# Optimization experiments

Measured on AMD Instinct MI355X. Metric: run time of the kernel, lower is better.

Reference implementation:

```python
import jax, jax.numpy as jnp
import numpy as np

A, B, NB = 100_000, 200_000, 6      # atoms, directed bonds, max neighbors
FA, FB, H = 133, 147, 256            # atom fdim, bond fdim, hidden
M, DEPTH = 5_000, 4                  # molecules, message-passing depth


def setup_inputs() -> dict:
    key = jax.random.key(0)
    ks = jax.random.split(key, 12)
    f_atoms = jax.random.normal(ks[0], (A, FA), jnp.float32)
    f_bonds = jax.random.normal(ks[1], (B, FB), jnp.float32)
    a2b = jax.random.randint(ks[2], (A, NB), 0, B, dtype=jnp.int32)
    b2a = jax.random.randint(ks[3], (B,), 0, A, dtype=jnp.int32)
    b2revb = jax.random.randint(ks[4], (B,), 0, B, dtype=jnp.int32)
    # weights (bias=False per args.bias, except W_o which always has bias)
    W_ia = jax.random.normal(ks[5], (FA, H), jnp.float32) / np.sqrt(FA)
    W_ib = jax.random.normal(ks[6], (FB, H), jnp.float32) / np.sqrt(FB)
    W_h = jax.random.normal(ks[7], (DEPTH - 1, H, H), jnp.float32) / np.sqrt(H)
    W_o = jax.random.normal(ks[8], (H, H), jnp.float32) / np.sqrt(H)
    b_o = jax.random.normal(ks[9], (H,), jnp.float32) * 0.01
    W_lr = jax.random.normal(ks[10], (3 * H, H), jnp.float32) / np.sqrt(3 * H)
    # ragged molecule sizes summing exactly to A (avg 20 atoms/mol)
    rng = np.random.default_rng(0)
    sizes = (A // M) + rng.integers(-5, 6, M)
    sizes[-1] += A - sizes.sum()
    sizes = jnp.asarray(sizes, jnp.int32)
    return dict(f_atoms=f_atoms, f_bonds=f_bonds, W_ia=W_ia, W_ib=W_ib,
                W_h=W_h, W_o=W_o, b_o=b_o, W_lr=W_lr,
                a2b=a2b, b2a=b2a, b2revb=b2revb, sizes=sizes)


def _sum_max_agg(message_bond, a2b):
    nei = message_bond[a2b]                 # [A, NB, H] gather
    return nei.sum(axis=1) * nei.max(axis=1)


def reference(f_atoms, f_bonds, W_ia, W_ib, W_h, W_o, b_o, W_lr,
              a2b, b2a, b2revb, sizes):
    input_atom = jax.nn.relu(f_atoms @ W_ia)    # [A, H]
    message_atom = input_atom
    input_bond = jax.nn.relu(f_bonds @ W_ib)    # [B, H]
    message_bond = input_bond
    for d in range(DEPTH - 1):
        agg = _sum_max_agg(message_bond, a2b)          # [A, H]
        message_atom = message_atom + agg
        rev = message_bond[b2revb]                     # [B, H]
        message_bond = message_atom[b2a] - rev
        message_bond = jax.nn.relu(input_bond + message_bond @ W_h[d])
        # dropout p=0.0 -> identity
    agg = _sum_max_agg(message_bond, a2b)              # [A, H]
    agg = jnp.concatenate([agg, message_atom, input_atom], axis=1) @ W_lr
    atom_hiddens = jax.nn.relu(agg @ W_o + b_o)        # [A, H]
    # ragged per-molecule mean pooling (a_scope)
    mol_ids = jnp.repeat(jnp.arange(M), sizes, total_repeat_length=A)
    sums = jax.ops.segment_sum(atom_hiddens, mol_ids, num_segments=M)
    mol_vecs = sums / sizes[:, None].astype(atom_hiddens.dtype)
    return mol_vecs                                    # [M, H]
```

## Files before the change

### kernel.cpp

```cpp
#include <hip/hip_runtime.h>


typedef _Float16 f16;
typedef f16 f16x4 __attribute__((ext_vector_type(4)));
typedef __attribute__((ext_vector_type(8))) short bh8;
typedef __attribute__((ext_vector_type(4))) float f32x4;

#define MB_SCALE 0.000244140625f
#define MB_INV   4096.0f
#define AGG_INV  16777216.0f

__device__ __forceinline__ unsigned short f2bf_rne(float f) {
    unsigned u = __float_as_uint(f);
    unsigned r = (u + 0x7fffu + ((u >> 16) & 1u)) >> 16;
    return (unsigned short)r;
}
__device__ __forceinline__ float bfu2f(unsigned short u) {
    return __uint_as_float(((unsigned)u) << 16);
}
__device__ __forceinline__ f32x4 mfma16(bh8 a, bh8 b, f32x4 c) {
    return __builtin_amdgcn_mfma_f32_16x16x32_bf16(a, b, c, 0, 0, 0);
}

__global__ __launch_bounds__(256) void wprep_kernel(
    const float* __restrict__ Wia, const float* __restrict__ Wib,
    const float* __restrict__ Wh,  const float* __restrict__ Wlr,
    const float* __restrict__ Wo,  short* __restrict__ ws)
{
    short* WiaT_hi = ws;
    short* WiaT_lo = ws + 40960;
    short* WibT_hi = ws + 81920;
    short* WibT_lo = ws + 122880;
    short* WhT_hi  = ws + 163840;
    short* WhT_lo  = ws + 360448;
    short* WlrT_hi = ws + 557056;
    short* WlrT_lo = ws + 753664;
    short* WoT_hi  = ws + 950272;
    short* WoT_lo  = ws + 1015808;

    int idx = blockIdx.x * 256 + threadIdx.x;
    float v; short *ph, *pl; int o;
    if (idx < 40960) {
        int n = idx / 160, k = idx - n * 160;
        v = (k < 133) ? Wia[(size_t)k * 256 + n] : 0.f;
        ph = WiaT_hi; pl = WiaT_lo; o = idx;
    } else if (idx < 81920) {
        int j = idx - 40960;
        int n = j / 160, k = j - n * 160;
        v = (k < 147) ? Wib[(size_t)k * 256 + n] : 0.f;
        ph = WibT_hi; pl = WibT_lo; o = j;
    } else if (idx < 278528) {
        int j = idx - 81920;
        int d = j >> 16, rem = j & 65535, n = rem >> 8, k = rem & 255;
        v = Wh[(size_t)d * 65536 + (size_t)k * 256 + n];
        ph = WhT_hi; pl = WhT_lo; o = j;
    } else if (idx < 475136) {
        int j = idx - 278528;
        int n = j / 768, k = j - n * 768;
        v = Wlr[(size_t)k * 256 + n];
        ph = WlrT_hi; pl = WlrT_lo; o = j;
    } else if (idx < 540672) {
        int j = idx - 475136;
        int n = j >> 8, k = j & 255;
        v = Wo[(size_t)k * 256 + n];
        ph = WoT_hi; pl = WoT_lo; o = j;
    } else return;
    unsigned short hb = f2bf_rne(v);
    ph[o] = (short)hb;
    pl[o] = (short)f2bf_rne(v - bfu2f(hb));
}

template <int KPAD, int SRC, int EPI>
__global__ __launch_bounds__(256) void mfma_gemm(
    const void* __restrict__ a0, const void* __restrict__ a1,
    const void* __restrict__ a2,
    const short* __restrict__ Bhi, const short* __restrict__ Blo,
    const float* __restrict__ bias, void* __restrict__ outv,
    int M, int Kact)
{
    __shared__ short As_hi[128 * 40];
    __shared__ short As_lo[(SRC == 2) ? 8 : 128 * 40];

    const int tid  = threadIdx.x;
    const int lane = tid & 63;
    const int w    = tid >> 6;
    const int wm   = (w >> 1) * 64;
    const int wn   = (w & 1) * 64;
    const int row0 = blockIdx.x * 128;
    const int colb = blockIdx.y * 128;

    const int sm = tid >> 1;
    const int sk = (tid & 1) * 16;
    const int fm = lane & 15;
    const int fk = (lane >> 4) * 8;

    int grow = row0 + sm; if (grow > M - 1) grow = M - 1;

    f32x4 acc[4][4];
#pragma unroll
    for (int i = 0; i < 4; ++i)
#pragma unroll
        for (int j = 0; j < 4; ++j) {
            f32x4 z = {0.f, 0.f, 0.f, 0.f};
            acc[i][j] = z;
        }

    for (int k0 = 0; k0 < KPAD; k0 += 32) {
        __syncthreads();
        if (SRC == 0) {
            const float* xrow = (const float*)a0 + (size_t)grow * Kact;
            bh8 h0, h1, l0, l1;
#pragma unroll
            for (int j = 0; j < 8; ++j) {
                int kc = k0 + sk + j;
                float v = (kc < Kact) ? xrow[kc] : 0.f;
                unsigned short hb = f2bf_rne(v);
                h0[j] = (short)hb; l0[j] = (short)f2bf_rne(v - bfu2f(hb));
                int kc2 = kc + 8;
                float v2 = (kc2 < Kact) ? xrow[kc2] : 0.f;
                unsigned short hb2 = f2bf_rne(v2);
                h1[j] = (short)hb2; l1[j] = (short)f2bf_rne(v2 - bfu2f(hb2));
            }
            int base = sm * 40 + sk;
            *(bh8*)&As_hi[base] = h0; *(bh8*)&As_hi[base + 8] = h1;
            *(bh8*)&As_lo[base] = l0; *(bh8*)&As_lo[base + 8] = l1;
        } else if (SRC == 1) {
            int base = sm * 40 + sk;
            if (k0 < 512) {
                const float* src = (k0 < 256) ? (const float*)a0 : (const float*)a1;
                int kl = k0 & 255;
                const float4* p = (const float4*)(src + (size_t)grow * 256 + kl + sk);
                float va[16];
#pragma unroll
                for (int q = 0; q < 4; ++q) {
                    float4 f = p[q];
                    va[q * 4 + 0] = f.x; va[q * 4 + 1] = f.y;
                    va[q * 4 + 2] = f.z; va[q * 4 + 3] = f.w;
                }
                bh8 h0, h1, l0, l1;
#pragma unroll
                for (int j = 0; j < 8; ++j) {
                    unsigned short hb = f2bf_rne(va[j]);
                    h0[j] = (short)hb; l0[j] = (short)f2bf_rne(va[j] - bfu2f(hb));
                    unsigned short hb2 = f2bf_rne(va[8 + j]);
                    h1[j] = (short)hb2; l1[j] = (short)f2bf_rne(va[8 + j] - bfu2f(hb2));
                }
                *(bh8*)&As_hi[base] = h0; *(bh8*)&As_hi[base + 8] = h1;
                *(bh8*)&As_lo[base] = l0; *(bh8*)&As_lo[base + 8] = l1;
            } else {
                const short* ia = (const short*)a2 + (size_t)grow * 256 + (k0 - 512) + sk;
                bh8 z;
#pragma unroll
                for (int j = 0; j < 8; ++j) z[j] = 0;
                *(bh8*)&As_hi[base]     = *(const bh8*)ia;
                *(bh8*)&As_hi[base + 8] = *(const bh8*)(ia + 8);
                *(bh8*)&As_lo[base] = z; *(bh8*)&As_lo[base + 8] = z;
            }
        } else {
            const short* xr = (const short*)a0 + (size_t)grow * 256 + k0 + sk;
            int base = sm * 40 + sk;
            *(bh8*)&As_hi[base]     = *(const bh8*)xr;
            *(bh8*)&As_hi[base + 8] = *(const bh8*)(xr + 8);
        }
        __syncthreads();

        bh8 bhf[4], blf[4];
#pragma unroll
        for (int nt = 0; nt < 4; ++nt) {
            int n = colb + wn + nt * 16 + fm;
            size_t off = (size_t)n * KPAD + k0 + fk;
            bhf[nt] = *(const bh8*)(Bhi + off);
            blf[nt] = *(const bh8*)(Blo + off);
        }
#pragma unroll
        for (int mt = 0; mt < 4; ++mt) {
            int abase = (wm + mt * 16 + fm) * 40 + fk;
            bh8 ah = *(const bh8*)&As_hi[abase];
#pragma unroll
            for (int nt = 0; nt < 4; ++nt) {
                acc[mt][nt] = mfma16(ah, bhf[nt], acc[mt][nt]);
                acc[mt][nt] = mfma16(ah, blf[nt], acc[mt][nt]);
            }
            if (SRC != 2) {
                bh8 al = *(const bh8*)&As_lo[abase];
#pragma unroll
                for (int nt = 0; nt < 4; ++nt)
                    acc[mt][nt] = mfma16(al, bhf[nt], acc[mt][nt]);
            }
        }
    }

#pragma unroll
    for (int mt = 0; mt < 4; ++mt) {
        int rbase = row0 + wm + mt * 16 + (lane >> 4) * 4;
#pragma unroll
        for (int nt = 0; nt < 4; ++nt) {
            int col = colb + wn + nt * 16 + fm;
            float bc = (EPI == 4) ? bias[col] : 0.f;
#pragma unroll
            for (int r = 0; r < 4; ++r) {
                int row = rbase + r;
                if (row < M) {
                    size_t o = (size_t)row * 256 + col;
                    float v = acc[mt][nt][r];
                    if (EPI == 0)      ((float*)outv)[o] = fmaxf(v, 0.f);
                    else if (EPI == 1) ((unsigned short*)outv)[o] = f2bf_rne(fmaxf(v, 0.f));
                    else if (EPI == 2) ((f16*)outv)[o] = (f16)(fmaxf(v, 0.f) * MB_SCALE);
                    else if (EPI == 3) ((unsigned short*)outv)[o] = f2bf_rne(v);
                    else               ((float*)outv)[o] = fmaxf(v + bc, 0.f);
                }
            }
        }
    }
}

__global__ __launch_bounds__(256) void bond_mfma_kernel(
    const float* __restrict__ FB,
    const short* __restrict__ WibT_hi, const short* __restrict__ WibT_lo,
    const short* __restrict__ WhT_hi,  const short* __restrict__ WhT_lo,
    const float* __restrict__ matom, const f16* __restrict__ mb_old,
    const int* __restrict__ b2a, const int* __restrict__ b2revb,
    f16* __restrict__ mb_new, int M)
{
    __shared__ short As_hi[128 * 40];
    __shared__ short As_lo[128 * 40];

    const int tid  = threadIdx.x;
    const int lane = tid & 63;
    const int w    = tid >> 6;
    const int wm   = (w >> 1) * 64;
    const int wn   = (w & 1) * 64;
    const int row0 = blockIdx.x * 128;
    const int colb = blockIdx.y * 128;

    const int sm = tid >> 1;
    const int sk = (tid & 1) * 16;

    int grow = row0 + sm; if (grow > M - 1) grow = M - 1;
    const float* frow = FB + (size_t)grow * 147;
    const float* arow = matom + (size_t)b2a[grow] * 256;
    const f16*   rrow = mb_old + (size_t)b2revb[grow] * 256;

    const int fm = lane & 15;
    const int fk = (lane >> 4) * 8;

    f32x4 acc[4][4];
#pragma unroll
    for (int i = 0; i < 4; ++i)
#pragma unroll
        for (int j = 0; j < 4; ++j) {
            f32x4 z = {0.f, 0.f, 0.f, 0.f};
            acc[i][j] = z;
        }

    for (int k0 = 0; k0 < 160; k0 += 32) {
        __syncthreads();
        {
            bh8 h0, h1, l0, l1;
#pragma unroll
            for (int j = 0; j < 8; ++j) {
                int kc = k0 + sk + j;
                float v = (kc < 147) ? frow[kc] : 0.f;
                unsigned short hb = f2bf_rne(v);
                h0[j] = (short)hb; l0[j] = (short)f2bf_rne(v - bfu2f(hb));
                int kc2 = kc + 8;
                float v2 = (kc2 < 147) ? frow[kc2] : 0.f;
                unsigned short hb2 = f2bf_rne(v2);
                h1[j] = (short)hb2; l1[j] = (short)f2bf_rne(v2 - bfu2f(hb2));
            }
            int base = sm * 40 + sk;
            *(bh8*)&As_hi[base] = h0; *(bh8*)&As_hi[base + 8] = h1;
            *(bh8*)&As_lo[base] = l0; *(bh8*)&As_lo[base + 8] = l1;
        }
        __syncthreads();

        bh8 bhf[4], blf[4];
#pragma unroll
        for (int nt = 0; nt < 4; ++nt) {
            int n = colb + wn + nt * 16 + fm;
            size_t off = (size_t)n * 160 + k0 + fk;
            bhf[nt] = *(const bh8*)(WibT_hi + off);
            blf[nt] = *(const bh8*)(WibT_lo + off);
        }
#pragma unroll
        for (int mt = 0; mt < 4; ++mt) {
            int abase = (wm + mt * 16 + fm) * 40 + fk;
            bh8 ah = *(const bh8*)&As_hi[abase];
            bh8 al = *(const bh8*)&As_lo[abase];
#pragma unroll
            for (int nt = 0; nt < 4; ++nt) {
                acc[mt][nt] = mfma16(ah, bhf[nt], acc[mt][nt]);
                acc[mt][nt] = mfma16(ah, blf[nt], acc[mt][nt]);
                acc[mt][nt] = mfma16(al, bhf[nt], acc[mt][nt]);
            }
        }
    }

#pragma unroll
    for (int i = 0; i < 4; ++i)
#pragma unroll
        for (int j = 0; j < 4; ++j)
#pragma unroll
            for (int r = 0; r < 4; ++r)
                acc[i][j][r] = fmaxf(acc[i][j][r], 0.f);

    for (int k0 = 0; k0 < 256; k0 += 32) {
        __syncthreads();
        {
            float va[16];
            const float4* ap = (const float4*)(arow + k0 + sk);
            const f16x4*  rp = (const f16x4*)(rrow + k0 + sk);
#pragma unroll
            for (int q = 0; q < 4; ++q) {
                float4 a = ap[q]; f16x4 r = rp[q];
                va[q * 4 + 0] = fmaf(-MB_INV, (float)r[0], a.x);
                va[q * 4 + 1] = fmaf(-MB_INV, (float)r[1], a.y);
                va[q * 4 + 2] = fmaf(-MB_INV, (float)r[2], a.z);
                va[q * 4 + 3] = fmaf(-MB_INV, (float)r[3], a.w);
            }
            bh8 h0, h1, l0, l1;
#pragma unroll
            for (int j = 0; j < 8; ++j) {
                unsigned short hb = f2bf_rne(va[j]);
                h0[j] = (short)hb; l0[j] = (short)f2bf_rne(va[j] - bfu2f(hb));
                unsigned short hb2 = f2bf_rne(va[8 + j]);
                h1[j] = (short)hb2; l1[j] = (short)f2bf_rne(va[8 + j] - bfu2f(hb2));
            }
            int base = sm * 40 + sk;
            *(bh8*)&As_hi[base] = h0; *(bh8*)&As_hi[base + 8] = h1;
            *(bh8*)&As_lo[base] = l0; *(bh8*)&As_lo[base + 8] = l1;
        }
        __syncthreads();

        bh8 bhf[4], blf[4];
#pragma unroll
        for (int nt = 0; nt < 4; ++nt) {
            int n = colb + wn + nt * 16 + fm;
            size_t off = (size_t)n * 256 + k0 + fk;
            bhf[nt] = *(const bh8*)(WhT_hi + off);
            blf[nt] = *(const bh8*)(WhT_lo + off);
        }
#pragma unroll
        for (int mt = 0; mt < 4; ++mt) {
            int abase = (wm + mt * 16 + fm) * 40 + fk;
            bh8 ah = *(const bh8*)&As_hi[abase];
            bh8 al = *(const bh8*)&As_lo[abase];
#pragma unroll
            for (int nt = 0; nt < 4; ++nt) {
                acc[mt][nt] = mfma16(ah, bhf[nt], acc[mt][nt]);
                acc[mt][nt] = mfma16(ah, blf[nt], acc[mt][nt]);
                acc[mt][nt] = mfma16(al, bhf[nt], acc[mt][nt]);
            }
        }
    }

#pragma unroll
    for (int mt = 0; mt < 4; ++mt) {
        int rbase = row0 + wm + mt * 16 + (lane >> 4) * 4;
#pragma unroll
        for (int nt = 0; nt < 4; ++nt) {
            int col = colb + wn + nt * 16 + fm;
#pragma unroll
            for (int r = 0; r < 4; ++r) {
                int row = rbase + r;
                if (row < M)
                    mb_new[(size_t)row * 256 + col] =
                        (f16)(fmaxf(acc[mt][nt][r], 0.f) * MB_SCALE);
            }
        }
    }
}

__global__ __launch_bounds__(256) void agg_kernel(
    const f16* __restrict__ mb, const int* __restrict__ a2b,
    float* __restrict__ matom, float* __restrict__ agg_out, int A)
{
    const int a = blockIdx.x;
    const int h = threadIdx.x;
    const int* nb = a2b + (size_t)a * 6;
    int i0 = nb[0], i1 = nb[1], i2 = nb[2], i3 = nb[3], i4 = nb[4], i5 = nb[5];
    float v0 = (float)mb[(size_t)i0 * 256 + h];
    float v1 = (float)mb[(size_t)i1 * 256 + h];
    float v2 = (float)mb[(size_t)i2 * 256 + h];
    float v3 = (float)mb[(size_t)i3 * 256 + h];
    float v4 = (float)mb[(size_t)i4 * 256 + h];
    float v5 = (float)mb[(size_t)i5 * 256 + h];
    float s = v0 + v1 + v2 + v3 + v4 + v5;
    float mx = fmaxf(fmaxf(fmaxf(v0, v1), fmaxf(v2, v3)), fmaxf(v4, v5));
    float g = AGG_INV * s * mx;
    size_t idx = (size_t)a * 256 + h;
    if (agg_out) agg_out[idx] = g;
    else         matom[idx] += g;
}

__global__ __launch_bounds__(256) void scan_kernel(
    const int* __restrict__ sizes, int* __restrict__ offsets, int M)
{
    __shared__ int part[256];
    const int t = threadIdx.x;
    const int chunk = (M + 255) / 256;
    int begin = t * chunk;
    int end = begin + chunk; if (end > M) end = M;
    int s = 0;
    for (int i = begin; i < end && i < M; ++i) s += sizes[i];
    part[t] = s;
    __syncthreads();
    for (int off = 1; off < 256; off <<= 1) {
        int v = (t >= off) ? part[t - off] : 0;
        __syncthreads();
        part[t] += v;
        __syncthreads();
    }
    int run = part[t] - s;
    for (int i = begin; i < end && i < M; ++i) { offsets[i] = run; run += sizes[i]; }
}

__global__ __launch_bounds__(256) void pool_kernel(
    const float* __restrict__ hid, const int* __restrict__ offsets,
    const int* __restrict__ sizes, float* __restrict__ out, int M, int A)
{
    const int m = blockIdx.x;
    const int h = threadIdx.x;
    int e = offsets[m];
    int sz = sizes[m];
    int start = e < A ? e : A;          if (start < 0) start = 0;
    int stop  = e + sz; if (stop > A) stop = A; if (stop < 0) stop = 0;
    float s = 0.f;
    for (int i = start; i < stop; ++i)
        s += hid[(size_t)i * 256 + h];
    out[(size_t)m * 256 + h] = s / (float)sz;
}

extern "C" void kernel_launch(void* const* d_in, const int* in_sizes, int n_in,
                              void* d_out, int out_size, void* d_ws, size_t ws_size,
                              hipStream_t stream)
{
    const float* f_atoms = (const float*)d_in[0];
    const float* f_bonds = (const float*)d_in[1];
    const float* W_ia    = (const float*)d_in[2];
    const float* W_ib    = (const float*)d_in[3];
    const float* W_h     = (const float*)d_in[4];
    const float* W_o     = (const float*)d_in[5];
    const float* b_o     = (const float*)d_in[6];
    const float* W_lr    = (const float*)d_in[7];
    const int*   a2b     = (const int*)d_in[8];
    const int*   b2a     = (const int*)d_in[9];
    const int*   b2revb  = (const int*)d_in[10];
    const int*   sizes   = (const int*)d_in[11];
    float* out = (float*)d_out;

    const int An = 100000, Bn = 200000, Mm = 5000;
    const size_t ABYTES = (size_t)An * 256 * 4;
    const size_t BBYTES = (size_t)Bn * 256 * 2;

    int*   offsets = (int*)d_ws;
    float* matom   = (float*)((char*)d_ws + 32768);
    f16*   mb0     = (f16*)((char*)matom + ABYTES);
    f16*   mb1     = (f16*)((char*)mb0 + BBYTES);
    short* wsplit  = (short*)((char*)mb1 + BBYTES);

    short* WiaT_hi = wsplit;
    short* WiaT_lo = wsplit + 40960;
    short* WibT_hi = wsplit + 81920;
    short* WibT_lo = wsplit + 122880;
    short* WhT_hi  = wsplit + 163840;
    short* WhT_lo  = wsplit + 360448;
    short* WlrT_hi = wsplit + 557056;
    short* WlrT_lo = wsplit + 753664;
    short* WoT_hi  = wsplit + 950272;
    short* WoT_lo  = wsplit + 1015808;

    dim3 blk(256);
    dim3 gA((An + 127) / 128, 2);
    dim3 gB((Bn + 127) / 128, 2);

    wprep_kernel<<<2112, blk, 0, stream>>>(W_ia, W_ib, W_h, W_lr, W_o, wsplit);

    mfma_gemm<160, 0, 0><<<gA, blk, 0, stream>>>(
        f_atoms, nullptr, nullptr, WiaT_hi, WiaT_lo, nullptr, matom, An, 133);
    mfma_gemm<160, 0, 2><<<gB, blk, 0, stream>>>(
        f_bonds, nullptr, nullptr, WibT_hi, WibT_lo, nullptr, mb0, Bn, 147);

    f16* cur = mb0; f16* nxt = mb1;
    for (int d = 0; d < 3; ++d) {
        agg_kernel<<<An, blk, 0, stream>>>(cur, a2b, matom, (float*)nullptr, An);
        bond_mfma_kernel<<<gB, blk, 0, stream>>>(
            f_bonds, WibT_hi, WibT_lo,
            WhT_hi + (size_t)d * 65536, WhT_lo + (size_t)d * 65536,
            matom, cur, b2a, b2revb, nxt, Bn);
        f16* t = cur; cur = nxt; nxt = t;
    }

    float* aggbuf = (float*)mb0;
    agg_kernel<<<An, blk, 0, stream>>>(cur, a2b, matom, aggbuf, An);

    unsigned short* iatom = (unsigned short*)mb1;
    unsigned short* t1    = (unsigned short*)((char*)mb1 + 51200000);
    mfma_gemm<160, 0, 1><<<gA, blk, 0, stream>>>(
        f_atoms, nullptr, nullptr, WiaT_hi, WiaT_lo, nullptr, iatom, An, 133);

    mfma_gemm<768, 1, 3><<<gA, blk, 0, stream>>>(
        aggbuf, matom, iatom, WlrT_hi, WlrT_lo, nullptr, t1, An, 768);

    float* hid = (float*)mb0;
    mfma_gemm<256, 2, 4><<<gA, blk, 0, stream>>>(
        t1, nullptr, nullptr, WoT_hi, WoT_lo, b_o, hid, An, 256);

    scan_kernel<<<1, 256, 0, stream>>>(sizes, offsets, Mm);
    pool_kernel<<<Mm, blk, 0, stream>>>(hid, offsets, sizes, out, Mm, An);
}
```

Before: 2.253 ms.

## Double-buffer LDS in bond kernel and vectorize agg kernel per-wave

The bond message kernel merges its two K loops into one 13-step loop with double-buffered LDS tiles. The next tile's global gather is issued before the current MFMAs and written to the other buffer afterwards, so each step needs one barrier instead of two and load latency overlaps compute. The aggregation kernel now handles four atoms per block, one wave each, using 4-wide half loads and float4 stores instead of one scalar per thread. The cost is double the LDS use and more live registers for the prefetched values, which may reduce occupancy.

```diff
diff --git a/kernel.cpp b/kernel.cpp
--- a/kernel.cpp
+++ b/kernel.cpp
@@ -222,8 +222,8 @@
     const int* __restrict__ b2a, const int* __restrict__ b2revb,
     f16* __restrict__ mb_new, int M)
 {
-    __shared__ short As_hi[128 * 40];
-    __shared__ short As_lo[128 * 40];
+    __shared__ short As_hi[2][128 * 40];
+    __shared__ short As_lo[2][128 * 40];
 
     const int tid  = threadIdx.x;
     const int lane = tid & 63;
@@ -235,15 +235,14 @@
 
     const int sm = tid >> 1;
     const int sk = (tid & 1) * 16;
+    const int fm = lane & 15;
+    const int fk = (lane >> 4) * 8;
 
     int grow = row0 + sm; if (grow > M - 1) grow = M - 1;
     const float* frow = FB + (size_t)grow * 147;
     const float* arow = matom + (size_t)b2a[grow] * 256;
     const f16*   rrow = mb_old + (size_t)b2revb[grow] * 256;
 
-    const int fm = lane & 15;
-    const int fk = (lane >> 4) * 8;
-
     f32x4 acc[4][4];
 #pragma unroll
     for (int i = 0; i < 4; ++i)
@@ -253,61 +252,16 @@
             acc[i][j] = z;
         }
 
-    for (int k0 = 0; k0 < 160; k0 += 32) {
-        __syncthreads();
-        {
-            bh8 h0, h1, l0, l1;
-#pragma unroll
-            for (int j = 0; j < 8; ++j) {
+    auto load_src = [&](int it, float va[16]) {
+        if (it < 5) {
+            int k0 = it * 32;
+#pragma unroll
+            for (int j = 0; j < 16; ++j) {
                 int kc = k0 + sk + j;
-                float v = (kc < 147) ? frow[kc] : 0.f;
-                unsigned short hb = f2bf_rne(v);
-                h0[j] = (short)hb; l0[j] = (short)f2bf_rne(v - bfu2f(hb));
-                int kc2 = kc + 8;
-                float v2 = (kc2 < 147) ? frow[kc2] : 0.f;
-                unsigned short hb2 = f2bf_rne(v2);
-                h1[j] = (short)hb2; l1[j] = (short)f2bf_rne(v2 - bfu2f(hb2));
-            }
-            int base = sm * 40 + sk;
-            *(bh8*)&As_hi[base] = h0; *(bh8*)&As_hi[base + 8] = h1;
-            *(bh8*)&As_lo[base] = l0; *(bh8*)&As_lo[base + 8] = l1;
-        }
-        __syncthreads();
-
-        bh8 bhf[4], blf[4];
-#pragma unroll
-        for (int nt = 0; nt < 4; ++nt) {
-            int n = colb + wn + nt * 16 + fm;
-            size_t off = (size_t)n * 160 + k0 + fk;
-            bhf[nt] = *(const bh8*)(WibT_hi + off);
-            blf[nt] = *(const bh8*)(WibT_lo + off);
-        }
-#pragma unroll
-        for (int mt = 0; mt < 4; ++mt) {
-            int abase = (wm + mt * 16 + fm) * 40 + fk;
-            bh8 ah = *(const bh8*)&As_hi[abase];
-            bh8 al = *(const bh8*)&As_lo[abase];
-#pragma unroll
-            for (int nt = 0; nt < 4; ++nt) {
-                acc[mt][nt] = mfma16(ah, bhf[nt], acc[mt][nt]);
-                acc[mt][nt] = mfma16(ah, blf[nt], acc[mt][nt]);
-                acc[mt][nt] = mfma16(al, bhf[nt], acc[mt][nt]);
-            }
-        }
-    }
-
-#pragma unroll
-    for (int i = 0; i < 4; ++i)
-#pragma unroll
-        for (int j = 0; j < 4; ++j)
-#pragma unroll
-            for (int r = 0; r < 4; ++r)
-                acc[i][j][r] = fmaxf(acc[i][j][r], 0.f);
-
-    for (int k0 = 0; k0 < 256; k0 += 32) {
-        __syncthreads();
-        {
-            float va[16];
+                va[j] = (kc < 147) ? frow[kc] : 0.f;
+            }
+        } else {
+            int k0 = (it - 5) * 32;
             const float4* ap = (const float4*)(arow + k0 + sk);
             const f16x4*  rp = (const f16x4*)(rrow + k0 + sk);
 #pragma unroll
@@ -318,33 +272,59 @@
                 va[q * 4 + 2] = fmaf(-MB_INV, (float)r[2], a.z);
                 va[q * 4 + 3] = fmaf(-MB_INV, (float)r[3], a.w);
             }
-            bh8 h0, h1, l0, l1;
-#pragma unroll
-            for (int j = 0; j < 8; ++j) {
-                unsigned short hb = f2bf_rne(va[j]);
-                h0[j] = (short)hb; l0[j] = (short)f2bf_rne(va[j] - bfu2f(hb));
-                unsigned short hb2 = f2bf_rne(va[8 + j]);
-                h1[j] = (short)hb2; l1[j] = (short)f2bf_rne(va[8 + j] - bfu2f(hb2));
-            }
-            int base = sm * 40 + sk;
-            *(bh8*)&As_hi[base] = h0; *(bh8*)&As_hi[base + 8] = h1;
-            *(bh8*)&As_lo[base] = l0; *(bh8*)&As_lo[base + 8] = l1;
-        }
-        __syncthreads();
+        }
+    };
+    auto write_lds = [&](int buf, const float va[16]) {
+        bh8 h0, h1, l0, l1;
+#pragma unroll
+        for (int j = 0; j < 8; ++j) {
+            unsigned short hb = f2bf_rne(va[j]);
+            h0[j] = (short)hb; l0[j] = (short)f2bf_rne(va[j] - bfu2f(hb));
+            unsigned short hb2 = f2bf_rne(va[8 + j]);
+            h1[j] = (short)hb2; l1[j] = (short)f2bf_rne(va[8 + j] - bfu2f(hb2));
+        }
+        int base = sm * 40 + sk;
+        *(bh8*)&As_hi[buf][base] = h0; *(bh8*)&As_hi[buf][base + 8] = h1;
+        *(bh8*)&As_lo[buf][base] = l0; *(bh8*)&As_lo[buf][base + 8] = l1;
+    };
+
+    {
+        float va[16];
+        load_src(0, va);
+        write_lds(0, va);
+    }
+    __syncthreads();
+
+    for (int it = 0; it < 13; ++it) {
+        const int buf = it & 1;
+        float vnext[16];
+        if (it + 1 < 13) load_src(it + 1, vnext);
 
         bh8 bhf[4], blf[4];
-#pragma unroll
-        for (int nt = 0; nt < 4; ++nt) {
-            int n = colb + wn + nt * 16 + fm;
-            size_t off = (size_t)n * 256 + k0 + fk;
-            bhf[nt] = *(const bh8*)(WhT_hi + off);
-            blf[nt] = *(const bh8*)(WhT_lo + off);
+        if (it < 5) {
+            int k0 = it * 32;
+#pragma unroll
+            for (int nt = 0; nt < 4; ++nt) {
+                int n = colb + wn + nt * 16 + fm;
+                size_t off = (size_t)n * 160 + k0 + fk;
+                bhf[nt] = *(const bh8*)(WibT_hi + off);
+                blf[nt] = *(const bh8*)(WibT_lo + off);
+            }
+        } else {
+            int k0 = (it - 5) * 32;
+#pragma unroll
+            for (int nt = 0; nt < 4; ++nt) {
+                int n = colb + wn + nt * 16 + fm;
+                size_t off = (size_t)n * 256 + k0 + fk;
+                bhf[nt] = *(const bh8*)(WhT_hi + off);
+                blf[nt] = *(const bh8*)(WhT_lo + off);
+            }
         }
 #pragma unroll
         for (int mt = 0; mt < 4; ++mt) {
             int abase = (wm + mt * 16 + fm) * 40 + fk;
-            bh8 ah = *(const bh8*)&As_hi[abase];
-            bh8 al = *(const bh8*)&As_lo[abase];
+            bh8 ah = *(const bh8*)&As_hi[buf][abase];
+            bh8 al = *(const bh8*)&As_lo[buf][abase];
 #pragma unroll
             for (int nt = 0; nt < 4; ++nt) {
                 acc[mt][nt] = mfma16(ah, bhf[nt], acc[mt][nt]);
@@ -352,6 +332,19 @@
                 acc[mt][nt] = mfma16(al, bhf[nt], acc[mt][nt]);
             }
         }
+
+        if (it == 4) {
+#pragma unroll
+            for (int i = 0; i < 4; ++i)
+#pragma unroll
+                for (int j = 0; j < 4; ++j)
+#pragma unroll
+                    for (int r = 0; r < 4; ++r)
+                        acc[i][j][r] = fmaxf(acc[i][j][r], 0.f);
+        }
+
+        if (it + 1 < 13) write_lds(buf ^ 1, vnext);
+        __syncthreads();
     }
 
 #pragma unroll
@@ -375,22 +368,36 @@
     const f16* __restrict__ mb, const int* __restrict__ a2b,
     float* __restrict__ matom, float* __restrict__ agg_out, int A)
 {
-    const int a = blockIdx.x;
-    const int h = threadIdx.x;
+    const int g    = threadIdx.x >> 6;
+    const int lane = threadIdx.x & 63;
+    const int a = blockIdx.x * 4 + g;
+    if (a >= A) return;
     const int* nb = a2b + (size_t)a * 6;
     int i0 = nb[0], i1 = nb[1], i2 = nb[2], i3 = nb[3], i4 = nb[4], i5 = nb[5];
-    float v0 = (float)mb[(size_t)i0 * 256 + h];
-    float v1 = (float)mb[(size_t)i1 * 256 + h];
-    float v2 = (float)mb[(size_t)i2 * 256 + h];
-    float v3 = (float)mb[(size_t)i3 * 256 + h];
-    float v4 = (float)mb[(size_t)i4 * 256 + h];
-    float v5 = (float)mb[(size_t)i5 * 256 + h];
-    float s = v0 + v1 + v2 + v3 + v4 + v5;
-    float mx = fmaxf(fmaxf(fmaxf(v0, v1), fmaxf(v2, v3)), fmaxf(v4, v5));
-    float g = AGG_INV * s * mx;
-    size_t idx = (size_t)a * 256 + h;
-    if (agg_out) agg_out[idx] = g;
-    else         matom[idx] += g;
+    const size_t co = (size_t)lane * 4;
+    f16x4 v0 = *(const f16x4*)(mb + (size_t)i0 * 256 + co);
+    f16x4 v1 = *(const f16x4*)(mb + (size_t)i1 * 256 + co);
+    f16x4 v2 = *(const f16x4*)(mb + (size_t)i2 * 256 + co);
+    f16x4 v3 = *(const f16x4*)(mb + (size_t)i3 * 256 + co);
+    f16x4 v4 = *(const f16x4*)(mb + (size_t)i4 * 256 + co);
+    f16x4 v5 = *(const f16x4*)(mb + (size_t)i5 * 256 + co);
+    float gva[4];
+#pragma unroll
+    for (int c = 0; c < 4; ++c) {
+        float f0 = (float)v0[c], f1 = (float)v1[c], f2 = (float)v2[c];
+        float f3 = (float)v3[c], f4 = (float)v4[c], f5 = (float)v5[c];
+        float s  = f0 + f1 + f2 + f3 + f4 + f5;
+        float mx = fmaxf(fmaxf(fmaxf(f0, f1), fmaxf(f2, f3)), fmaxf(f4, f5));
+        gva[c] = AGG_INV * s * mx;
+    }
+    size_t o = (size_t)a * 256 + co;
+    if (agg_out) {
+        *(float4*)(agg_out + o) = make_float4(gva[0], gva[1], gva[2], gva[3]);
+    } else {
+        float4 m = *(const float4*)(matom + o);
+        m.x += gva[0]; m.y += gva[1]; m.z += gva[2]; m.w += gva[3];
+        *(float4*)(matom + o) = m;
+    }
 }
 
 __global__ __launch_bounds__(256) void scan_kernel(
@@ -483,7 +490,7 @@
 
     f16* cur = mb0; f16* nxt = mb1;
     for (int d = 0; d < 3; ++d) {
-        agg_kernel<<<An, blk, 0, stream>>>(cur, a2b, matom, (float*)nullptr, An);
+        agg_kernel<<<(An + 3) / 4, blk, 0, stream>>>(cur, a2b, matom, (float*)nullptr, An);
         bond_mfma_kernel<<<gB, blk, 0, stream>>>(
             f_bonds, WibT_hi, WibT_lo,
             WhT_hi + (size_t)d * 65536, WhT_lo + (size_t)d * 65536,
@@ -492,7 +499,7 @@
     }
 
     float* aggbuf = (float*)mb0;
-    agg_kernel<<<An, blk, 0, stream>>>(cur, a2b, matom, aggbuf, An);
+    agg_kernel<<<(An + 3) / 4, blk, 0, stream>>>(cur, a2b, matom, aggbuf, An);
 
     unsigned short* iatom = (unsigned short*)mb1;
     unsigned short* t1    = (unsigned short*)((char*)mb1 + 51200000);
```

Measured after the change: 2.674 ms. 1.19x slower.
